# Kernel optimization log

Measured on AMD Instinct MI355X. Metric: run time of the kernel, lower is better.

Reference implementation:

```python
import jax, jax.numpy as jnp
import numpy as np

QUEST_DIM = 768
C, X, Y = 2048, 19, 19
B = 64

def setup_inputs() -> dict:
    key = jax.random.key(0)
    k1, k2, k3, k4 = jax.random.split(key, 4)
    text_fts = jax.random.normal(k1, (B, QUEST_DIM), dtype=jnp.float32)
    img_fts = jax.random.normal(k2, (B, C, X, Y), dtype=jnp.float32)
    # Linear params (PyTorch nn.Linear: y = x @ W.T + b)
    bound = 1.0 / np.sqrt(QUEST_DIM)
    W = jax.random.uniform(k3, (C, QUEST_DIM), minval=-bound, maxval=bound, dtype=jnp.float32)
    b = jax.random.uniform(k4, (C,), minval=-bound, maxval=bound, dtype=jnp.float32)
    return {"text_fts": text_fts, "img_fts": img_fts, "W": W, "b": b}

def reference(text_fts, img_fts, W, b):
    batch = text_fts.shape[0]
    q = text_fts @ W.T + b                      # [B, C]
    img_flat = img_fts.reshape(batch, C, X * Y) # [B, C, S]
    sims = jnp.einsum('bc,bcs->bs', q, img_flat)  # dot over channel dim
    weights = jax.nn.softmax(sims, axis=1)        # softmax over spatial locations
    final_ans = jnp.einsum('bcs,bs->bc', img_flat, weights)  # weighted pooling
    return final_ans
```

## Files before the change

kernel.cpp:

```cpp
#include <hip/hip_runtime.h>
#include <math.h>

#define Bsz  64
#define Cch  2048
#define Kdim 768
#define Ssp  361
#define CPB  16
#define REGF (CPB * Ssp)
#define NFULL 22
#define NTAIL 36
#define NCG   (Cch / CPB)

__device__ __forceinline__ void dma16(const float* g, float* l) {
    __builtin_amdgcn_global_load_lds(
        (const __attribute__((address_space(1))) void*)(g),
        (__attribute__((address_space(3))) void*)(l),
        16, 0, 0);
}

__device__ __forceinline__ void stage_slice(const float* region, float* lds,
                                            int wv, int lane) {
    for (int i = wv; i < NFULL + 1; i += 6) {
        if (i < NFULL || lane < NTAIL)
            dma16(region + i * 256 + lane * 4, lds + i * 256);
    }
    asm volatile("s_waitcnt vmcnt(0)" ::: "memory");
}

__global__ __launch_bounds__(256) void k_qgemm(
    const float* __restrict__ text, const float* __restrict__ W,
    const float* __restrict__ bias, float* __restrict__ qT)
{
    const int lane = threadIdx.x & 63;
    const int wv   = threadIdx.x >> 6;
    const int c0   = blockIdx.x * 8 + wv * 2;
    const int b0   = blockIdx.y * 8;

    const float4* wA = (const float4*)(W + (size_t)c0 * Kdim);
    const float4* wB = (const float4*)(W + (size_t)(c0 + 1) * Kdim);
    const float4 a0 = wA[lane*3+0], a1 = wA[lane*3+1], a2 = wA[lane*3+2];
    const float4 g0 = wB[lane*3+0], g1 = wB[lane*3+1], g2 = wB[lane*3+2];
    const float biasA = bias[c0], biasB = bias[c0 + 1];

    for (int b = b0; b < b0 + 8; b += 2) {
        const float4* tp = (const float4*)(text + (size_t)b * Kdim);
        const float4* up = (const float4*)(text + (size_t)(b + 1) * Kdim);
        const float4 t0 = tp[lane*3+0], t1 = tp[lane*3+1], t2 = tp[lane*3+2];
        const float4 u0 = up[lane*3+0], u1 = up[lane*3+1], u2 = up[lane*3+2];

        float r00 = a0.x*t0.x + a0.y*t0.y + a0.z*t0.z + a0.w*t0.w
                  + a1.x*t1.x + a1.y*t1.y + a1.z*t1.z + a1.w*t1.w
                  + a2.x*t2.x + a2.y*t2.y + a2.z*t2.z + a2.w*t2.w;
        float r10 = g0.x*t0.x + g0.y*t0.y + g0.z*t0.z + g0.w*t0.w
                  + g1.x*t1.x + g1.y*t1.y + g1.z*t1.z + g1.w*t1.w
                  + g2.x*t2.x + g2.y*t2.y + g2.z*t2.z + g2.w*t2.w;
        float r01 = a0.x*u0.x + a0.y*u0.y + a0.z*u0.z + a0.w*u0.w
                  + a1.x*u1.x + a1.y*u1.y + a1.z*u1.z + a1.w*u1.w
                  + a2.x*u2.x + a2.y*u2.y + a2.z*u2.z + a2.w*u2.w;
        float r11 = g0.x*u0.x + g0.y*u0.y + g0.z*u0.z + g0.w*u0.w
                  + g1.x*u1.x + g1.y*u1.y + g1.z*u1.z + g1.w*u1.w
                  + g2.x*u2.x + g2.y*u2.y + g2.z*u2.z + g2.w*u2.w;
        #pragma unroll
        for (int off = 32; off; off >>= 1) {
            r00 += __shfl_xor(r00, off);
            r10 += __shfl_xor(r10, off);
            r01 += __shfl_xor(r01, off);
            r11 += __shfl_xor(r11, off);
        }
        if (lane == 0) {
            qT[(size_t)c0 * Bsz + b]           = r00 + biasA;
            qT[(size_t)(c0 + 1) * Bsz + b]     = r10 + biasB;
            qT[(size_t)c0 * Bsz + b + 1]       = r01 + biasA;
            qT[(size_t)(c0 + 1) * Bsz + b + 1] = r11 + biasB;
        }
    }
}

__global__ __launch_bounds__(384) void k_sims(
    const float* __restrict__ img, const float* __restrict__ qT,
    float* __restrict__ sims_part)
{
    const int b  = blockIdx.x;
    const int cg = blockIdx.y;
    const int tid = threadIdx.x;
    const int lane = tid & 63;
    const int wv   = tid >> 6;

    __shared__ float lds[REGF];
    __shared__ float qL[CPB];

    if (tid < CPB) qL[tid] = qT[(size_t)(cg * CPB + tid) * Bsz + b];

    const float* region = img + ((size_t)b * Cch + (size_t)cg * CPB) * Ssp;
    stage_slice(region, lds, wv, lane);
    __syncthreads();

    if (tid < Ssp) {
        float acc = 0.f;
        #pragma unroll
        for (int c = 0; c < CPB; c++)
            acc += qL[c] * lds[c * Ssp + tid];
        sims_part[((size_t)b * NCG + cg) * Ssp + tid] = acc;
    }
}

__global__ __launch_bounds__(384) void k_wts(
    const float* __restrict__ sims_part, float* __restrict__ wts)
{
    const int b   = blockIdx.x;
    const int tid = threadIdx.x;
    const int lane = tid & 63;
    const int wv   = tid >> 6;

    __shared__ float red[6];

    float s0 = -1e30f;
    if (tid < Ssp) {
        const float* sp = sims_part + (size_t)b * NCG * Ssp + tid;
        float a = 0.f;
        for (int g0 = 0; g0 < 128; g0 += 16) {
            float v[16];
            #pragma unroll
            for (int j = 0; j < 16; j++) v[j] = sp[(size_t)(g0 + j) * Ssp];
            #pragma unroll
            for (int j = 0; j < 16; j++) a += v[j];
        }
        s0 = a;
    }

    float m = s0;
    #pragma unroll
    for (int off = 32; off; off >>= 1) m = fmaxf(m, __shfl_xor(m, off));
    if (lane == 0) red[wv] = m;
    __syncthreads();
    m = red[0];
    #pragma unroll
    for (int w = 1; w < 6; w++) m = fmaxf(m, red[w]);
    __syncthreads();

    const float e0 = (tid < Ssp) ? __expf(s0 - m) : 0.f;
    float l = e0;
    #pragma unroll
    for (int off = 32; off; off >>= 1) l += __shfl_xor(l, off);
    if (lane == 0) red[wv] = l;
    __syncthreads();
    l = red[0] + red[1] + red[2] + red[3] + red[4] + red[5];

    if (tid < Ssp)
        wts[(size_t)b * Ssp + tid] = e0 / l;
}

__global__ __launch_bounds__(256) void k_pool(
    const float* __restrict__ img, const float* __restrict__ wts,
    float* __restrict__ out)
{
    const int b    = blockIdx.x;
    const int cg   = blockIdx.y;
    const int tid  = threadIdx.x;
    const int lane = tid & 63;
    const int wv   = tid >> 6;

    __shared__ float wL[Ssp];
    for (int s = tid; s < Ssp; s += 256)
        wL[s] = wts[(size_t)b * Ssp + s];
    __syncthreads();

    float wreg[6];
    #pragma unroll
    for (int k = 0; k < 6; k++) {
        const int s = lane + 64 * k;
        wreg[k] = (s < Ssp) ? wL[s] : 0.f;
    }

    const float* base = img + ((size_t)b * Cch + (size_t)cg * 128) * Ssp;
    const int c0 = wv * 32;

    for (int i = 0; i < 32; i += 4) {
        const float* r0 = base + (size_t)(c0 + i + 0) * Ssp;
        const float* r1 = base + (size_t)(c0 + i + 1) * Ssp;
        const float* r2 = base + (size_t)(c0 + i + 2) * Ssp;
        const float* r3 = base + (size_t)(c0 + i + 3) * Ssp;

        float a0 = 0.f, a1 = 0.f, a2 = 0.f, a3 = 0.f;
        #pragma unroll
        for (int k = 0; k < 6; k++) {
            const int s = lane + 64 * k;
            const bool ok = (s < Ssp);
            const float v0 = ok ? r0[s] : 0.f;
            const float v1 = ok ? r1[s] : 0.f;
            const float v2 = ok ? r2[s] : 0.f;
            const float v3 = ok ? r3[s] : 0.f;
            a0 += v0 * wreg[k];
            a1 += v1 * wreg[k];
            a2 += v2 * wreg[k];
            a3 += v3 * wreg[k];
        }
        #pragma unroll
        for (int off = 32; off; off >>= 1) {
            a0 += __shfl_xor(a0, off);
            a1 += __shfl_xor(a1, off);
            a2 += __shfl_xor(a2, off);
            a3 += __shfl_xor(a3, off);
        }
        if (lane == 0) {
            float* o = out + (size_t)b * Cch + (size_t)cg * 128 + c0 + i;
            o[0] = a0; o[1] = a1; o[2] = a2; o[3] = a3;
        }
    }
}

extern "C" void kernel_launch(void* const* d_in, const int* in_sizes, int n_in,
                              void* d_out, int out_size, void* d_ws, size_t ws_size,
                              hipStream_t stream) {
    const float* text = (const float*)d_in[0];
    const float* img  = (const float*)d_in[1];
    const float* W    = (const float*)d_in[2];
    const float* bias = (const float*)d_in[3];
    float* out = (float*)d_out;

    float* qT        = (float*)d_ws;
    float* sims_part = qT + (size_t)Cch * Bsz;
    float* wts       = sims_part + (size_t)Bsz * NCG * Ssp;

    k_qgemm<<<dim3(256, 8),   256, 0, stream>>>(text, W, bias, qT);
    k_sims <<<dim3(Bsz, NCG), 384, 0, stream>>>(img, qT, sims_part);
    k_wts  <<<dim3(Bsz),      384, 0, stream>>>(sims_part, wts);
    k_pool <<<dim3(Bsz, 16),  256, 0, stream>>>(img, wts, out);
}
```

Measured before the change: 319.0 us.

## Fuse query GEMM into sims kernel and double pool grid parallelism

Removes the separate q-projection kernel and computes each block's 16 query values inside k_sims: 384 threads each take a partial dot product over the 768 text dimensions while the image slice DMA into LDS is in flight, then the partials are reduced in shared memory. This drops one kernel launch and the qT round trip through global memory, and overlaps the GEMM loads with the image staging. In exchange, W and text rows are re-read by every batch block (64x redundant GEMM work). Separately, k_pool now uses 64 channels per block with twice as many blocks, for more parallelism.

```diff
diff --git a/kernel.cpp b/kernel.cpp
--- a/kernel.cpp
+++ b/kernel.cpp
@@ -18,66 +18,9 @@
         16, 0, 0);
 }
 
-__device__ __forceinline__ void stage_slice(const float* region, float* lds,
-                                            int wv, int lane) {
-    for (int i = wv; i < NFULL + 1; i += 6) {
-        if (i < NFULL || lane < NTAIL)
-            dma16(region + i * 256 + lane * 4, lds + i * 256);
-    }
-    asm volatile("s_waitcnt vmcnt(0)" ::: "memory");
-}
-
-__global__ __launch_bounds__(256) void k_qgemm(
+__global__ __launch_bounds__(384) void k_sims(
     const float* __restrict__ text, const float* __restrict__ W,
-    const float* __restrict__ bias, float* __restrict__ qT)
-{
-    const int lane = threadIdx.x & 63;
-    const int wv   = threadIdx.x >> 6;
-    const int c0   = blockIdx.x * 8 + wv * 2;
-    const int b0   = blockIdx.y * 8;
-
-    const float4* wA = (const float4*)(W + (size_t)c0 * Kdim);
-    const float4* wB = (const float4*)(W + (size_t)(c0 + 1) * Kdim);
-    const float4 a0 = wA[lane*3+0], a1 = wA[lane*3+1], a2 = wA[lane*3+2];
-    const float4 g0 = wB[lane*3+0], g1 = wB[lane*3+1], g2 = wB[lane*3+2];
-    const float biasA = bias[c0], biasB = bias[c0 + 1];
-
-    for (int b = b0; b < b0 + 8; b += 2) {
-        const float4* tp = (const float4*)(text + (size_t)b * Kdim);
-        const float4* up = (const float4*)(text + (size_t)(b + 1) * Kdim);
-        const float4 t0 = tp[lane*3+0], t1 = tp[lane*3+1], t2 = tp[lane*3+2];
-        const float4 u0 = up[lane*3+0], u1 = up[lane*3+1], u2 = up[lane*3+2];
-
-        float r00 = a0.x*t0.x + a0.y*t0.y + a0.z*t0.z + a0.w*t0.w
-                  + a1.x*t1.x + a1.y*t1.y + a1.z*t1.z + a1.w*t1.w
-                  + a2.x*t2.x + a2.y*t2.y + a2.z*t2.z + a2.w*t2.w;
-        float r10 = g0.x*t0.x + g0.y*t0.y + g0.z*t0.z + g0.w*t0.w
-                  + g1.x*t1.x + g1.y*t1.y + g1.z*t1.z + g1.w*t1.w
-                  + g2.x*t2.x + g2.y*t2.y + g2.z*t2.z + g2.w*t2.w;
-        float r01 = a0.x*u0.x + a0.y*u0.y + a0.z*u0.z + a0.w*u0.w
-                  + a1.x*u1.x + a1.y*u1.y + a1.z*u1.z + a1.w*u1.w
-                  + a2.x*u2.x + a2.y*u2.y + a2.z*u2.z + a2.w*u2.w;
-        float r11 = g0.x*u0.x + g0.y*u0.y + g0.z*u0.z + g0.w*u0.w
-                  + g1.x*u1.x + g1.y*u1.y + g1.z*u1.z + g1.w*u1.w
-                  + g2.x*u2.x + g2.y*u2.y + g2.z*u2.z + g2.w*u2.w;
-        #pragma unroll
-        for (int off = 32; off; off >>= 1) {
-            r00 += __shfl_xor(r00, off);
-            r10 += __shfl_xor(r10, off);
-            r01 += __shfl_xor(r01, off);
-            r11 += __shfl_xor(r11, off);
-        }
-        if (lane == 0) {
-            qT[(size_t)c0 * Bsz + b]           = r00 + biasA;
-            qT[(size_t)(c0 + 1) * Bsz + b]     = r10 + biasB;
-            qT[(size_t)c0 * Bsz + b + 1]       = r01 + biasA;
-            qT[(size_t)(c0 + 1) * Bsz + b + 1] = r11 + biasB;
-        }
-    }
-}
-
-__global__ __launch_bounds__(384) void k_sims(
-    const float* __restrict__ img, const float* __restrict__ qT,
+    const float* __restrict__ bias, const float* __restrict__ img,
     float* __restrict__ sims_part)
 {
     const int b  = blockIdx.x;
@@ -86,13 +29,40 @@
     const int lane = tid & 63;
     const int wv   = tid >> 6;
 
-    __shared__ float lds[REGF];
+    __shared__ __align__(16) float lds[REGF];
+    __shared__ float qpart[16 * 24];
     __shared__ float qL[CPB];
 
-    if (tid < CPB) qL[tid] = qT[(size_t)(cg * CPB + tid) * Bsz + b];
+    const float* region = img + ((size_t)b * Cch + (size_t)cg * CPB) * Ssp;
+    for (int i = wv; i < NFULL + 1; i += 6) {
+        if (i < NFULL || lane < NTAIL)
+            dma16(region + i * 256 + lane * 4, lds + i * 256);
+    }
 
-    const float* region = img + ((size_t)b * Cch + (size_t)cg * CPB) * Ssp;
-    stage_slice(region, lds, wv, lane);
+    {
+        const int qc = tid / 24;
+        const int qj = tid - qc * 24;
+        const float4* wr = (const float4*)(W + (size_t)(cg * CPB + qc) * Kdim);
+        const float4* tr = (const float4*)(text + (size_t)b * Kdim);
+        float acc = 0.f;
+        #pragma unroll
+        for (int t = 0; t < 8; t++) {
+            const float4 w4 = wr[qj + 24 * t];
+            const float4 t4 = tr[qj + 24 * t];
+            acc += w4.x * t4.x + w4.y * t4.y + w4.z * t4.z + w4.w * t4.w;
+        }
+        qpart[qc * 24 + qj] = acc;
+    }
+
+    asm volatile("s_waitcnt vmcnt(0)" ::: "memory");
+    __syncthreads();
+
+    if (tid < CPB) {
+        float q = bias[cg * CPB + tid];
+        #pragma unroll
+        for (int j = 0; j < 24; j++) q += qpart[tid * 24 + j];
+        qL[tid] = q;
+    }
     __syncthreads();
 
     if (tid < Ssp) {
@@ -172,10 +142,10 @@
         wreg[k] = (s < Ssp) ? wL[s] : 0.f;
     }
 
-    const float* base = img + ((size_t)b * Cch + (size_t)cg * 128) * Ssp;
-    const int c0 = wv * 32;
+    const float* base = img + ((size_t)b * Cch + (size_t)cg * 64) * Ssp;
+    const int c0 = wv * 16;
 
-    for (int i = 0; i < 32; i += 4) {
+    for (int i = 0; i < 16; i += 4) {
         const float* r0 = base + (size_t)(c0 + i + 0) * Ssp;
         const float* r1 = base + (size_t)(c0 + i + 1) * Ssp;
         const float* r2 = base + (size_t)(c0 + i + 2) * Ssp;
@@ -203,7 +173,7 @@
             a3 += __shfl_xor(a3, off);
         }
         if (lane == 0) {
-            float* o = out + (size_t)b * Cch + (size_t)cg * 128 + c0 + i;
+            float* o = out + (size_t)b * Cch + (size_t)cg * 64 + c0 + i;
             o[0] = a0; o[1] = a1; o[2] = a2; o[3] = a3;
         }
     }
@@ -221,9 +191,9 @@
     float* qT        = (float*)d_ws;
     float* sims_part = qT + (size_t)Cch * Bsz;
     float* wts       = sims_part + (size_t)Bsz * NCG * Ssp;
+    (void)qT;
 
-    k_qgemm<<<dim3(256, 8),   256, 0, stream>>>(text, W, bias, qT);
-    k_sims <<<dim3(Bsz, NCG), 384, 0, stream>>>(img, qT, sims_part);
+    k_sims <<<dim3(Bsz, NCG), 384, 0, stream>>>(text, W, bias, img, sims_part);
     k_wts  <<<dim3(Bsz),      384, 0, stream>>>(sims_part, wts);
-    k_pool <<<dim3(Bsz, 16),  256, 0, stream>>>(img, wts, out);
+    k_pool <<<dim3(Bsz, 32),  256, 0, stream>>>(img, wts, out);
 }
```

After: 313.7 us. Within noise of the previous version (-1.7%).
